# Optimization experiments

Measured on AMD Instinct MI355X. Metric: run time of the kernel, lower is better.

The kernel has to match this reference:

```python
import jax, jax.numpy as jnp
import numpy as np

N_NODES = 100000
N_EDGES = 1600000
D_INPUT = 128
D_HIDDEN = 16
N_HEADS = 8
NCLASSES = 40
N_GRAPHS = 64
ALPHA = 0.2  # LeakyReLU negative slope
INIT = 0.01  # GAT_param_init uniform range


def setup_inputs() -> dict:
    key = jax.random.key(0)
    ks = jax.random.split(key, 7)
    x = jax.random.normal(ks[0], (N_NODES, D_INPUT), dtype=jnp.float32)
    edge_idx = jax.random.randint(ks[1], (2, N_EDGES), 0, N_NODES, dtype=jnp.int64)
    batch = jnp.sort(jax.random.randint(ks[2], (N_NODES,), 0, N_GRAPHS, dtype=jnp.int64))
    # layer1: d_input -> n_heads * d_hidden, concat aggregate
    W1 = jax.random.uniform(ks[3], (D_INPUT, N_HEADS * D_HIDDEN), dtype=jnp.float32, minval=-INIT, maxval=INIT)
    a1 = jax.random.uniform(ks[4], (N_HEADS, 2 * D_HIDDEN), dtype=jnp.float32, minval=-INIT, maxval=INIT)
    # layer2: n_heads*d_hidden -> nclasses, 1 head, mean aggregate
    W2 = jax.random.uniform(ks[5], (N_HEADS * D_HIDDEN, NCLASSES), dtype=jnp.float32, minval=-INIT, maxval=INIT)
    a2 = jax.random.uniform(ks[6], (1, 2 * NCLASSES), dtype=jnp.float32, minval=-INIT, maxval=INIT)
    return {"x": x, "W1": W1, "a1": a1, "W2": W2, "a2": a2, "edge_idx": edge_idx, "batch": batch}


def _gat_layer(x, W, a, n_heads, d_out, src, dst, aggregate):
    # x: [N, d_in]; W: [d_in, H*D]; a: [H, 2*D]
    n = x.shape[0]
    Wh = (x @ W).reshape(n, n_heads, d_out)                  # [N, H, D]
    e_src = jnp.einsum('nhd,hd->nh', Wh, a[:, :d_out])       # [N, H]
    e_dst = jnp.einsum('nhd,hd->nh', Wh, a[:, d_out:])       # [N, H]
    e = jax.nn.leaky_relu(e_src[src] + e_dst[dst], ALPHA)    # [E, H]
    # segment softmax over edges sharing the same destination node
    m = jax.ops.segment_max(e, dst, num_segments=n)          # [N, H]
    m = jnp.where(jnp.isfinite(m), m, 0.0)                   # nodes w/o in-edges
    ex = jnp.exp(e - m[dst])
    s = jax.ops.segment_sum(ex, dst, num_segments=n)
    att = ex / (s[dst] + 1e-16)                              # [E, H]
    # weighted scatter-aggregate of neighbor features
    out = jax.ops.segment_sum(att[:, :, None] * Wh[src], dst, num_segments=n)  # [N, H, D]
    if aggregate == 'concat':
        return out.reshape(n, n_heads * d_out)
    return out.mean(axis=1)


def reference(x, W1, a1, W2, a2, edge_idx, batch):
    # eval mode: F.dropout(training=False) is identity
    src, dst = edge_idx[0], edge_idx[1]
    h1 = _gat_layer(x, W1, a1, N_HEADS, D_HIDDEN, src, dst, 'concat')
    h1 = jax.nn.elu(h1)
    h2 = _gat_layer(h1, W2, a2, 1, NCLASSES, src, dst, 'mean')   # [N, nclasses]
    # global_mean_pool over graph ids
    sums = jax.ops.segment_sum(h2, batch, num_segments=N_GRAPHS)
    cnt = jax.ops.segment_sum(jnp.ones((h2.shape[0],), h2.dtype), batch, num_segments=N_GRAPHS)
    return sums / jnp.maximum(cnt, 1.0)[:, None]
```

## Files before the change

### kernel.cpp

```cpp
#include <hip/hip_runtime.h>
#include <hip/hip_bf16.h>

typedef unsigned short u16;
typedef unsigned int   u32;
typedef float f32x2 __attribute__((ext_vector_type(2)));
typedef float f32x4 __attribute__((ext_vector_type(4)));
typedef short bf16x8 __attribute__((ext_vector_type(8)));

static constexpr int NN = 100000;
static constexpr int NE = 1600000;
static constexpr int NG = 64;

static constexpr int BSH   = 8;
static constexpr int NBUCK = 391;
static constexpr int BCAP  = 5120;
static constexpr int PB    = 8;

__device__ __forceinline__ u16 bf16rte(float a) {
  u32 u = __builtin_bit_cast(u32, a);
  u = (u + 0x7FFFu + ((u >> 16) & 1u)) >> 16;
  return (u16)u;
}
__device__ __forceinline__ u32 bf16pair(float a, float b) {
  return (u32)bf16rte(a) | ((u32)bf16rte(b) << 16);
}
__device__ __forceinline__ float bflo(u32 u) { return __builtin_bit_cast(float, u << 16); }
__device__ __forceinline__ float bfhi(u32 u) { return __builtin_bit_cast(float, u & 0xFFFF0000u); }

__device__ __forceinline__ void pkfma(f32x2& a, f32x2 w2, u32 u) {
  f32x2 v;
  v.x = bflo(u); v.y = bfhi(u);
  asm("v_pk_fma_f32 %0, %1, %2, %0" : "+v"(a) : "v"(w2), "v"(v));
}

__global__ void k_prep(const float* __restrict__ W1, u16* __restrict__ wsTg,
                       const int* __restrict__ batch, int* __restrict__ gstart,
                       int* __restrict__ cur) {
  const int bid = blockIdx.x;
  if (bid < 64) {
    int idx = bid * 256 + threadIdx.x;
    int k = idx >> 7, c = idx & 127;
    wsTg[c * 128 + (((k >> 3) ^ (c & 7)) << 3) + (k & 7)] = bf16rte(W1[idx]);
  } else {
    int t = threadIdx.x;
    for (int i = t; i < NBUCK; i += 256) cur[i] = 0;
    if (t <= NG) {
      int lo = 0, hi = NN;
      while (lo < hi) { int mid = (lo + hi) >> 1; if (batch[mid] < t) lo = mid + 1; else hi = mid; }
      gstart[t] = lo;
    }
  }
}

__global__ __launch_bounds__(256) void k_gemm1(
    const float* __restrict__ x, const u16* __restrict__ wsTg, const float* __restrict__ a1,
    u16* __restrict__ Wh1b, float* __restrict__ es1, float* __restrict__ ed1)
{
  __shared__ u16 wsT[128][128];
  __shared__ u16 xsb[64][32];
  const int t = threadIdx.x;
  const int w = t >> 6, l = t & 63;
  const int rowBase = blockIdx.x * 64;

  {
    const uint4* src = (const uint4*)wsTg;
    uint4* dst = (uint4*)&wsT[0][0];
#pragma unroll
    for (int i = 0; i < 8; ++i) dst[t * 8 + i] = src[t * 8 + i];
  }

  f32x4 acc[4][2];
#pragma unroll
  for (int r = 0; r < 4; ++r)
#pragma unroll
    for (int cf = 0; cf < 2; ++cf) acc[r][cf] = (f32x4){0.f, 0.f, 0.f, 0.f};

  const int rr = t >> 2, cg = t & 3;
  const int grow_s = rowBase + rr;

  for (int kk0 = 0; kk0 < 128; kk0 += 32) {
    float4 v0 = make_float4(0.f, 0.f, 0.f, 0.f), v1 = v0;
    if (grow_s < NN) {
      v0 = *(const float4*)(&x[(size_t)grow_s * 128 + kk0 + cg * 8]);
      v1 = *(const float4*)(&x[(size_t)grow_s * 128 + kk0 + cg * 8 + 4]);
    }
    if (kk0) __syncthreads();
    {
      u32 p0 = bf16pair(v0.x, v0.y);
      u32 p1 = bf16pair(v0.z, v0.w);
      u32 p2 = bf16pair(v1.x, v1.y);
      u32 p3 = bf16pair(v1.z, v1.w);
      int sg = cg ^ ((rr >> 1) & 3);
      *(uint4*)(&xsb[rr][sg * 8]) = make_uint4(p0, p1, p2, p3);
    }
    __syncthreads();

    bf16x8 bfr[2];
#pragma unroll
    for (int cf = 0; cf < 2; ++cf) {
      int col = w * 32 + cf * 16 + (l & 15);
      int kg = (kk0 >> 3) + (l >> 4);
      bfr[cf] = *(const bf16x8*)(&wsT[col][(kg ^ (col & 7)) * 8]);
    }
#pragma unroll
    for (int r = 0; r < 4; ++r) {
      int row = r * 16 + (l & 15);
      int kg = l >> 4;
      bf16x8 afr = *(const bf16x8*)(&xsb[row][(kg ^ ((row >> 1) & 3)) * 8]);
#pragma unroll
      for (int cf = 0; cf < 2; ++cf)
        acc[r][cf] = __builtin_amdgcn_mfma_f32_16x16x32_bf16(afr, bfr[cf], acc[r][cf], 0, 0, 0);
    }
  }

  const int cl = l & 15;
  const int rq = l >> 4;
#pragma unroll
  for (int cf = 0; cf < 2; ++cf) {
    const int h = w * 2 + cf;
    const int gcol = w * 32 + cf * 16 + cl;
    const float as = a1[h * 32 + cl];
    const float ad = a1[h * 32 + 16 + cl];
#pragma unroll
    for (int r = 0; r < 4; ++r) {
#pragma unroll
      for (int i = 0; i < 4; ++i) {
        int grow = rowBase + r * 16 + rq * 4 + i;
        float wh = acc[r][cf][i];
        float ps = wh * as, pd = wh * ad;
        ps += __shfl_xor(ps, 1); ps += __shfl_xor(ps, 2);
        ps += __shfl_xor(ps, 4); ps += __shfl_xor(ps, 8);
        pd += __shfl_xor(pd, 1); pd += __shfl_xor(pd, 2);
        pd += __shfl_xor(pd, 4); pd += __shfl_xor(pd, 8);
        if (grow < NN) {
          Wh1b[(size_t)grow * 128 + gcol] = bf16rte(wh);
          if (cl == 0) { es1[grow * 8 + h] = ps; ed1[grow * 8 + h] = pd; }
        }
      }
    }
  }
}

__global__ __launch_bounds__(256) void k_bin(
    const int* __restrict__ src, const int* __restrict__ dst,
    int* __restrict__ cur, u32* __restrict__ ebuf)
{
  __shared__ int lcnt2[2][512];
  __shared__ int scn[512];
  __shared__ int goff[NBUCK];
  const int t = threadIdx.x;
  const int wp = (t >> 7) & 1;
  const int e0 = blockIdx.x * 4096;

  lcnt2[0][t] = 0; lcnt2[0][t + 256] = 0;
  lcnt2[1][t] = 0; lcnt2[1][t + 256] = 0;
  __syncthreads();

  u32 ent[16]; short bb[16], lp[16];
#pragma unroll
  for (int i = 0; i < 16; ++i) {
    int e = e0 + i * 256 + t;
    if (e < NE) {
      int s = src[e], d = dst[e];
      int b = d >> BSH;
      ent[i] = (u32)s | ((u32)(d & 255) << 20);
      bb[i] = (short)b;
      lp[i] = (short)atomicAdd(&lcnt2[wp][b], 1);
    } else bb[i] = -1;
  }
  __syncthreads();
  scn[t] = lcnt2[0][t] + lcnt2[1][t];
  scn[t + 256] = lcnt2[0][t + 256] + lcnt2[1][t + 256];
  __syncthreads();
  for (int d = 1; d < 512; d <<= 1) {
    int v0 = (t >= d) ? scn[t - d] : 0;
    int v1 = (t + 256 >= d) ? scn[t + 256 - d] : 0;
    __syncthreads();
    scn[t] += v0; scn[t + 256] += v1;
    __syncthreads();
  }
  for (int b = t; b < NBUCK; b += 256) {
    int excl = b ? scn[b - 1] : 0;
    int cnt = scn[b] - excl;
    if (cnt) goff[b] = b * BCAP + atomicAdd(&cur[b], cnt);
  }
  __syncthreads();
#pragma unroll
  for (int i = 0; i < 16; ++i) {
    if (bb[i] >= 0) {
      int b = bb[i];
      int g = goff[b] + (wp ? lcnt2[0][b] : 0) + lp[i];
      if (g < (b + 1) * BCAP) ebuf[g] = ent[i];
    }
  }
}

__global__ __launch_bounds__(256) void k_sort(
    const int* __restrict__ cur, u32* __restrict__ ebuf,
    int* __restrict__ offs, int* __restrict__ deg)
{
  __shared__ u32 ein[BCAP];
  __shared__ u32 eout[BCAP];
  __shared__ int nd[256];
  __shared__ int ncur[256];
  const int t = threadIdx.x;
  const int b = blockIdx.x;
  const int base = b * BCAP;
  int cnt = cur[b];
  if (cnt > BCAP) cnt = BCAP;
  const int nloc = min(256, NN - (b << BSH));

  for (int i = t; i < cnt; i += 256) ein[i] = ebuf[base + i];
  nd[t] = 0;
  __syncthreads();
  for (int i = t; i < cnt; i += 256) atomicAdd(&nd[ein[i] >> 20], 1);
  __syncthreads();
  const int myCnt = nd[t];
  for (int d = 1; d < 256; d <<= 1) {
    int v = (t >= d) ? nd[t - d] : 0;
    __syncthreads();
    nd[t] += v;
    __syncthreads();
  }
  const int excl = t ? nd[t - 1] : 0;
  ncur[t] = excl;
  if (t < nloc) {
    int node = (b << BSH) + t;
    offs[node] = base + excl;
    deg[node]  = myCnt;
  }
  __syncthreads();
  for (int i = t; i < cnt; i += 256) {
    u32 v = ein[i];
    int pos = atomicAdd(&ncur[v >> 20], 1);
    eout[pos] = v & 0xFFFFFu;
  }
  __syncthreads();
  for (int i = t; i < cnt; i += 256) ebuf[base + i] = eout[i];
}

__global__ __launch_bounds__(256, 8) void k_agg1(
    const u16* __restrict__ Wh1b, const float* __restrict__ es1, const float* __restrict__ ed1,
    const int* __restrict__ offs, const int* __restrict__ deg, const int* __restrict__ csr,
    u16* __restrict__ h1b)
{
  const int wid = threadIdx.x >> 6;
  const int lane = threadIdx.x & 63;
  const int n = blockIdx.x * 4 + wid;
  if (n >= NN) return;
  const int s0 = offs[n];
  const int nE = deg[n];
  const int g = lane >> 4;
  const int db = lane & 15;
  const int h = db >> 1;
  const float edv = ed1[n * 8 + h];

  f32x2 acc[4];
#pragma unroll
  for (int i = 0; i < 4; ++i) { acc[i].x = 0.f; acc[i].y = 0.f; }
  float ssum = 0.f;

  int c0 = 0;
  for (; c0 + 16 <= nE; c0 += 16) {
    int ss[4];
#pragma unroll
    for (int q = 0; q < 4; ++q) ss[q] = csr[s0 + c0 + q * 4 + g];
    float zz[4];
#pragma unroll
    for (int q = 0; q < 4; ++q) {
      float z = es1[ss[q] * 8 + h] + edv;
      zz[q] = (z > 0.f) ? z : 0.2f * z;
    }
    uint4 raw[4];
#pragma unroll
    for (int q = 0; q < 4; ++q)
      raw[q] = *(const uint4*)(Wh1b + (size_t)ss[q] * 128 + db * 8);
#pragma unroll
    for (int q = 0; q < 4; ++q) {
      const float ww = __expf(zz[q]);
      ssum += ww;
      f32x2 w2; w2.x = ww; w2.y = ww;
      pkfma(acc[0], w2, raw[q].x);
      pkfma(acc[1], w2, raw[q].y);
      pkfma(acc[2], w2, raw[q].z);
      pkfma(acc[3], w2, raw[q].w);
    }
  }
  if (c0 < nE) {
    int jj[4], ss[4];
#pragma unroll
    for (int q = 0; q < 4; ++q) {
      jj[q] = c0 + q * 4 + g;
      ss[q] = csr[s0 + (jj[q] < nE ? jj[q] : 0)];
    }
    float zz[4];
#pragma unroll
    for (int q = 0; q < 4; ++q) {
      float z = es1[ss[q] * 8 + h] + edv;
      zz[q] = (z > 0.f) ? z : 0.2f * z;
    }
#pragma unroll
    for (int q = 0; q < 4; ++q) {
      if (jj[q] < nE) {
        const uint4 raw = *(const uint4*)(Wh1b + (size_t)ss[q] * 128 + db * 8);
        const float ww = __expf(zz[q]);
        ssum += ww;
        f32x2 w2; w2.x = ww; w2.y = ww;
        pkfma(acc[0], w2, raw.x);
        pkfma(acc[1], w2, raw.y);
        pkfma(acc[2], w2, raw.z);
        pkfma(acc[3], w2, raw.w);
      }
    }
  }
#pragma unroll
  for (int i = 0; i < 4; ++i) {
    acc[i].x += __shfl_xor(acc[i].x, 16);
    acc[i].y += __shfl_xor(acc[i].y, 16);
    acc[i].x += __shfl_xor(acc[i].x, 32);
    acc[i].y += __shfl_xor(acc[i].y, 32);
  }
  ssum += __shfl_xor(ssum, 16);
  ssum += __shfl_xor(ssum, 32);

  if (g == 0) {
    float inv = 1.f / (ssum + 1e-16f);
    float o[8];
#pragma unroll
    for (int i = 0; i < 4; ++i) {
      float v0 = acc[i].x * inv;
      float v1 = acc[i].y * inv;
      o[2 * i]     = (v0 > 0.f) ? v0 : expm1f(v0);
      o[2 * i + 1] = (v1 > 0.f) ? v1 : expm1f(v1);
    }
    u32 p0 = bf16pair(o[0], o[1]);
    u32 p1 = bf16pair(o[2], o[3]);
    u32 p2 = bf16pair(o[4], o[5]);
    u32 p3 = bf16pair(o[6], o[7]);
    *(uint4*)(h1b + (size_t)n * 128 + db * 8) = make_uint4(p0, p1, p2, p3);
  }
}

__global__ __launch_bounds__(256) void k_gemm2(
    const u16* __restrict__ h1b, const float* __restrict__ W2,
    const float* __restrict__ a2,
    u16* __restrict__ Wh2b, float* __restrict__ es2, float* __restrict__ ed2)
{
  __shared__ float hs[128][36];
  __shared__ float w2s[32][40];
  const int t = threadIdx.x;
  const int rowBase = blockIdx.x * 128;
  const int cg = t & 3;
  const int rs = t >> 2;
  float acc[2][10];
#pragma unroll
  for (int r = 0; r < 2; ++r)
#pragma unroll
    for (int j = 0; j < 10; ++j) acc[r][j] = 0.f;

  for (int k0 = 0; k0 < 128; k0 += 32) {
#pragma unroll
    for (int p = 0; p < 2; ++p) {
      int idx = (p * 256 + t) * 8;
      int rr = idx >> 5, cc = idx & 31;
      int grow = rowBase + rr;
      uint4 hv = make_uint4(0u, 0u, 0u, 0u);
      if (grow < NN) hv = *(const uint4*)(h1b + (size_t)grow * 128 + k0 + cc);
      float2* dst = (float2*)&hs[rr][cc];
      dst[0] = make_float2(bflo(hv.x), bfhi(hv.x));
      dst[1] = make_float2(bflo(hv.y), bfhi(hv.y));
      dst[2] = make_float2(bflo(hv.z), bfhi(hv.z));
      dst[3] = make_float2(bflo(hv.w), bfhi(hv.w));
    }
#pragma unroll
    for (int p = 0; p < 5; ++p) {
      int idx = p * 256 + t;
      int kk = idx / 40, cc = idx % 40;
      w2s[kk][cc] = W2[(size_t)(k0 + kk) * 40 + cc];
    }
    __syncthreads();
#pragma unroll
    for (int k = 0; k < 32; ++k) {
      float a0 = hs[rs][k], a1v = hs[rs + 64][k];
#pragma unroll
      for (int j = 0; j < 10; ++j) {
        float b = w2s[k][cg * 10 + j];
        acc[0][j] = fmaf(a0, b, acc[0][j]);
        acc[1][j] = fmaf(a1v, b, acc[1][j]);
      }
    }
    __syncthreads();
  }
  float a2s[10], a2d[10];
#pragma unroll
  for (int j = 0; j < 10; ++j) {
    a2s[j] = a2[cg * 10 + j];
    a2d[j] = a2[40 + cg * 10 + j];
  }
#pragma unroll
  for (int rr = 0; rr < 2; ++rr) {
    int grow = rowBase + rs + rr * 64;
    float pes = 0.f, ped = 0.f;
#pragma unroll
    for (int j = 0; j < 10; ++j) {
      float v = acc[rr][j];
      pes = fmaf(v, a2s[j], pes);
      ped = fmaf(v, a2d[j], ped);
    }
    if (grow < NN) {
      u32* dst = (u32*)(Wh2b + (size_t)grow * 48 + cg * 10);
      dst[0] = bf16pair(acc[rr][0], acc[rr][1]);
      dst[1] = bf16pair(acc[rr][2], acc[rr][3]);
      dst[2] = bf16pair(acc[rr][4], acc[rr][5]);
      dst[3] = bf16pair(acc[rr][6], acc[rr][7]);
      dst[4] = bf16pair(acc[rr][8], acc[rr][9]);
    }
    pes += __shfl_xor(pes, 1); pes += __shfl_xor(pes, 2);
    ped += __shfl_xor(ped, 1); ped += __shfl_xor(ped, 2);
    if (cg == 0 && grow < NN) { es2[grow] = pes; ed2[grow] = ped; }
  }
}

__global__ __launch_bounds__(256, 8) void k_agg2(
    const u16* __restrict__ Wh2b, const float* __restrict__ es2, const float* __restrict__ ed2,
    const int* __restrict__ offs, const int* __restrict__ deg, const int* __restrict__ csr,
    u32* __restrict__ h2b)
{
  __shared__ float red[4][64][5];
  const int wid = threadIdx.x >> 6;
  const int lane = threadIdx.x & 63;
  const int n = blockIdx.x * 4 + wid;
  if (n >= NN) return;
  const int s0 = offs[n];
  const int nE = deg[n];
  const float edv = ed2[n];
  int e6 = lane / 10;
  const int r10 = lane - e6 * 10;
  const bool act = lane < 60;
  if (e6 > 5) e6 = 5;

  f32x2 acc0, acc1;
  acc0.x = acc0.y = acc1.x = acc1.y = 0.f;
  float ssum = 0.f;

  for (int c0 = 0; c0 < nE; c0 += 24) {
    int jj[4], ss[4];
#pragma unroll
    for (int q = 0; q < 4; ++q) {
      jj[q] = c0 + q * 6 + e6;
      ss[q] = csr[s0 + (jj[q] < nE ? jj[q] : 0)];
    }
    float zz[4];
#pragma unroll
    for (int q = 0; q < 4; ++q) {
      float z = es2[ss[q]] + edv;
      zz[q] = (z > 0.f) ? z : 0.2f * z;
    }
#pragma unroll
    for (int q = 0; q < 4; ++q) {
      if (act && jj[q] < nE) {
        const uint2 raw = *(const uint2*)(Wh2b + (size_t)ss[q] * 48 + r10 * 4);
        const float ww = __expf(zz[q]);
        ssum += ww;
        f32x2 w2; w2.x = ww; w2.y = ww;
        pkfma(acc0, w2, raw.x);
        pkfma(acc1, w2, raw.y);
      }
    }
  }
  red[wid][lane][0] = acc0.x; red[wid][lane][1] = acc0.y;
  red[wid][lane][2] = acc1.x; red[wid][lane][3] = acc1.y;
  red[wid][lane][4] = ssum;
  __builtin_amdgcn_wave_barrier();
  if (lane < 20) {
    const int rb = lane >> 1;
    const int eA = (lane & 1) * 2;
    float aA = 0.f, aB = 0.f, sm = 0.f;
#pragma unroll
    for (int g = 0; g < 6; ++g) {
      aA += red[wid][g * 10 + rb][eA];
      aB += red[wid][g * 10 + rb][eA + 1];
      sm += red[wid][g * 10][4];
    }
    float inv = 1.f / (sm + 1e-16f);
    h2b[(size_t)n * 20 + lane] = bf16pair(aA * inv, aB * inv);
  }
}

__global__ __launch_bounds__(256) void k_pool1(
    const u32* __restrict__ h2b, const int* __restrict__ gstart,
    float* __restrict__ partial)
{
  __shared__ float lds[25][10][4];
  const int g = blockIdx.x >> 3;
  const int p = blockIdx.x & 7;
  const int t = threadIdx.x;
  const int s0 = gstart[g], s1 = gstart[g + 1];
  const int len = s1 - s0;
  const int chunk = (len + PB - 1) / PB;
  const int start = s0 + p * chunk;
  const int end = min(start + chunk, s1);
  const int slot = t / 10, q = t - slot * 10;
  float4 acc = make_float4(0.f, 0.f, 0.f, 0.f);
  if (slot < 25) {
    for (int n = start + slot; n < end; n += 25) {
      const uint2 v = *(const uint2*)(&h2b[(size_t)n * 20 + q * 2]);
      acc.x += bflo(v.x); acc.y += bfhi(v.x);
      acc.z += bflo(v.y); acc.w += bfhi(v.y);
    }
    lds[slot][q][0] = acc.x; lds[slot][q][1] = acc.y;
    lds[slot][q][2] = acc.z; lds[slot][q][3] = acc.w;
  }
  __syncthreads();
  if (t < 40) {
    const int qq = t >> 2, e = t & 3;
    float s = 0.f;
#pragma unroll
    for (int sl = 0; sl < 25; ++sl) s += lds[sl][qq][e];
    partial[(size_t)blockIdx.x * 40 + t] = s;
  }
}

__global__ void k_pool2(const float* __restrict__ partial, const int* __restrict__ gstart,
                        float* __restrict__ out)
{
  const int g = blockIdx.x;
  const int d = threadIdx.x;
  if (d >= 40) return;
  float s = 0.f;
#pragma unroll
  for (int p = 0; p < PB; ++p) s += partial[(size_t)(g * PB + p) * 40 + d];
  int cnt = gstart[g + 1] - gstart[g];
  if (cnt < 1) cnt = 1;
  out[g * 40 + d] = s / (float)cnt;
}

extern "C" void kernel_launch(void* const* d_in, const int* in_sizes, int n_in,
                              void* d_out, int out_size, void* d_ws, size_t ws_size,
                              hipStream_t stream)
{
  const float* x   = (const float*)d_in[0];
  const float* W1  = (const float*)d_in[1];
  const float* a1  = (const float*)d_in[2];
  const float* W2  = (const float*)d_in[3];
  const float* a2  = (const float*)d_in[4];
  const int* eidx  = (const int*)d_in[5];
  const int* batch = (const int*)d_in[6];
  float* out = (float*)d_out;

  char* ws = (char*)d_ws;
  u16*   Wh1b = (u16*)(ws + 0);
  u16*   Wh2b = (u16*)(ws + 0);
  u32*   h2b  = (u32*)(ws + 9600000);
  u16*   h1b  = (u16*)(ws + 25600000);
  float* es1  = (float*)(ws + 51200000);
  float* ed1  = (float*)(ws + 54400000);
  float* es2  = (float*)(ws + 57600000);
  float* ed2  = (float*)(ws + 58000000);
  u32*   ebuf = (u32*)(ws + 58400000);
  int*   offs = (int*)(ws + 66407680);
  int*   deg  = (int*)(ws + 66807680);
  int*   cur  = (int*)(ws + 67207680);
  int*   gstart = (int*)(ws + 67209728);
  float* partial = (float*)(ws + 67210240);
  u16*   wsTg = (u16*)(ws + 67292160);

  const int* esrc = eidx;
  const int* edst = eidx + NE;

  k_prep<<<65, 256, 0, stream>>>(W1, wsTg, batch, gstart, cur);
  k_gemm1<<<(NN + 63) / 64, 256, 0, stream>>>(x, wsTg, a1, Wh1b, es1, ed1);
  k_bin<<<(NE + 4095) / 4096, 256, 0, stream>>>(esrc, edst, cur, ebuf);
  k_sort<<<NBUCK, 256, 0, stream>>>(cur, ebuf, offs, deg);
  k_agg1<<<(NN + 3) / 4, 256, 0, stream>>>(Wh1b, es1, ed1, offs, deg, (const int*)ebuf, h1b);
  k_gemm2<<<(NN + 127) / 128, 256, 0, stream>>>(h1b, W2, a2, Wh2b, es2, ed2);
  k_agg2<<<(NN + 3) / 4, 256, 0, stream>>>(Wh2b, es2, ed2, offs, deg, (const int*)ebuf, h2b);
  k_pool1<<<NG * PB, 256, 0, stream>>>(h2b, gstart, partial);
  k_pool2<<<NG, 64, 0, stream>>>(partial, gstart, out);
}
```

Before: 245.1 us.

## Fuse layer-2 projection into layer-1 aggregation kernel via LDS-resident W2

Merges the layer-1 aggregation with the layer-2 GEMM. Each wave now applies ELU to its node's aggregated features in registers and immediately multiplies them by a bf16-packed W2 staged in shared memory. It then reduces across lanes to produce Wh2, es2 and ed2 directly. This removes the bf16 h1 intermediate's global write and re-read, plus one kernel launch. In exchange, every block reloads 10 KB of packed W2 into LDS, and the occupancy hint on the fused kernel is relaxed.

Result: faster. 238.4 us (median of 2 runs) (-2.7%).

```diff
diff --git a/kernel.cpp b/kernel.cpp
--- a/kernel.cpp
+++ b/kernel.cpp
@@ -35,19 +35,28 @@
 
 __global__ void k_prep(const float* __restrict__ W1, u16* __restrict__ wsTg,
                        const int* __restrict__ batch, int* __restrict__ gstart,
-                       int* __restrict__ cur) {
+                       int* __restrict__ cur,
+                       const float* __restrict__ W2, u32* __restrict__ wsW2) {
   const int bid = blockIdx.x;
   if (bid < 64) {
     int idx = bid * 256 + threadIdx.x;
     int k = idx >> 7, c = idx & 127;
     wsTg[c * 128 + (((k >> 3) ^ (c & 7)) << 3) + (k & 7)] = bf16rte(W1[idx]);
-  } else {
+  } else if (bid == 64) {
     int t = threadIdx.x;
     for (int i = t; i < NBUCK; i += 256) cur[i] = 0;
     if (t <= NG) {
       int lo = 0, hi = NN;
       while (lo < hi) { int mid = (lo + hi) >> 1; if (batch[mid] < t) lo = mid + 1; else hi = mid; }
       gstart[t] = lo;
+    }
+  } else {
+    const int t = threadIdx.x;
+#pragma unroll
+    for (int i = 0; i < 10; ++i) {
+      int idx = t * 10 + i;
+      int pc = idx >> 7, d = idx & 127;
+      wsW2[idx] = bf16pair(W2[d * 40 + pc * 2], W2[d * 40 + pc * 2 + 1]);
     }
   }
 }
@@ -239,13 +248,20 @@
   for (int i = t; i < cnt; i += 256) ebuf[base + i] = eout[i];
 }
 
-__global__ __launch_bounds__(256, 8) void k_agg1(
+__global__ __launch_bounds__(256) void k_agg1g2(
     const u16* __restrict__ Wh1b, const float* __restrict__ es1, const float* __restrict__ ed1,
     const int* __restrict__ offs, const int* __restrict__ deg, const int* __restrict__ csr,
-    u16* __restrict__ h1b)
-{
-  const int wid = threadIdx.x >> 6;
-  const int lane = threadIdx.x & 63;
+    const u32* __restrict__ wsW2, const float* __restrict__ a2,
+    u16* __restrict__ Wh2b, float* __restrict__ es2, float* __restrict__ ed2)
+{
+  __shared__ u32 W2s[2560];
+  const int t = threadIdx.x;
+#pragma unroll
+  for (int i = 0; i < 10; ++i) W2s[t * 10 + i] = wsW2[t * 10 + i];
+  __syncthreads();
+
+  const int wid = t >> 6;
+  const int lane = t & 63;
   const int n = blockIdx.x * 4 + wid;
   if (n >= NN) return;
   const int s0 = offs[n];
@@ -323,101 +339,53 @@
   ssum += __shfl_xor(ssum, 16);
   ssum += __shfl_xor(ssum, 32);
 
-  if (g == 0) {
-    float inv = 1.f / (ssum + 1e-16f);
-    float o[8];
-#pragma unroll
-    for (int i = 0; i < 4; ++i) {
-      float v0 = acc[i].x * inv;
-      float v1 = acc[i].y * inv;
-      o[2 * i]     = (v0 > 0.f) ? v0 : expm1f(v0);
-      o[2 * i + 1] = (v1 > 0.f) ? v1 : expm1f(v1);
-    }
-    u32 p0 = bf16pair(o[0], o[1]);
-    u32 p1 = bf16pair(o[2], o[3]);
-    u32 p2 = bf16pair(o[4], o[5]);
-    u32 p3 = bf16pair(o[6], o[7]);
-    *(uint4*)(h1b + (size_t)n * 128 + db * 8) = make_uint4(p0, p1, p2, p3);
-  }
-}
-
-__global__ __launch_bounds__(256) void k_gemm2(
-    const u16* __restrict__ h1b, const float* __restrict__ W2,
-    const float* __restrict__ a2,
-    u16* __restrict__ Wh2b, float* __restrict__ es2, float* __restrict__ ed2)
-{
-  __shared__ float hs[128][36];
-  __shared__ float w2s[32][40];
-  const int t = threadIdx.x;
-  const int rowBase = blockIdx.x * 128;
-  const int cg = t & 3;
-  const int rs = t >> 2;
-  float acc[2][10];
-#pragma unroll
-  for (int r = 0; r < 2; ++r)
-#pragma unroll
-    for (int j = 0; j < 10; ++j) acc[r][j] = 0.f;
-
-  for (int k0 = 0; k0 < 128; k0 += 32) {
-#pragma unroll
-    for (int p = 0; p < 2; ++p) {
-      int idx = (p * 256 + t) * 8;
-      int rr = idx >> 5, cc = idx & 31;
-      int grow = rowBase + rr;
-      uint4 hv = make_uint4(0u, 0u, 0u, 0u);
-      if (grow < NN) hv = *(const uint4*)(h1b + (size_t)grow * 128 + k0 + cc);
-      float2* dst = (float2*)&hs[rr][cc];
-      dst[0] = make_float2(bflo(hv.x), bfhi(hv.x));
-      dst[1] = make_float2(bflo(hv.y), bfhi(hv.y));
-      dst[2] = make_float2(bflo(hv.z), bfhi(hv.z));
-      dst[3] = make_float2(bflo(hv.w), bfhi(hv.w));
-    }
+  const float inv = 1.f / (ssum + 1e-16f);
+  float hv[8];
+#pragma unroll
+  for (int i = 0; i < 4; ++i) {
+    float v0 = acc[i].x * inv;
+    float v1 = acc[i].y * inv;
+    hv[2 * i]     = (v0 > 0.f) ? v0 : expm1f(v0);
+    hv[2 * i + 1] = (v1 > 0.f) ? v1 : expm1f(v1);
+  }
+
+  float o[10];
+#pragma unroll
+  for (int j = 0; j < 10; ++j) o[j] = 0.f;
+#pragma unroll
+  for (int d = 0; d < 8; ++d) {
+    const float hvd = hv[d];
+    const int row = db * 8 + d;
 #pragma unroll
     for (int p = 0; p < 5; ++p) {
-      int idx = p * 256 + t;
-      int kk = idx / 40, cc = idx % 40;
-      w2s[kk][cc] = W2[(size_t)(k0 + kk) * 40 + cc];
-    }
-    __syncthreads();
-#pragma unroll
-    for (int k = 0; k < 32; ++k) {
-      float a0 = hs[rs][k], a1v = hs[rs + 64][k];
-#pragma unroll
-      for (int j = 0; j < 10; ++j) {
-        float b = w2s[k][cg * 10 + j];
-        acc[0][j] = fmaf(a0, b, acc[0][j]);
-        acc[1][j] = fmaf(a1v, b, acc[1][j]);
-      }
-    }
-    __syncthreads();
-  }
-  float a2s[10], a2d[10];
+      u32 pr = W2s[(g * 5 + p) * 128 + row];
+      o[2 * p]     = fmaf(hvd, bflo(pr), o[2 * p]);
+      o[2 * p + 1] = fmaf(hvd, bfhi(pr), o[2 * p + 1]);
+    }
+  }
 #pragma unroll
   for (int j = 0; j < 10; ++j) {
-    a2s[j] = a2[cg * 10 + j];
-    a2d[j] = a2[40 + cg * 10 + j];
-  }
-#pragma unroll
-  for (int rr = 0; rr < 2; ++rr) {
-    int grow = rowBase + rs + rr * 64;
+    o[j] += __shfl_xor(o[j], 1);
+    o[j] += __shfl_xor(o[j], 2);
+    o[j] += __shfl_xor(o[j], 4);
+    o[j] += __shfl_xor(o[j], 8);
+  }
+  if (db == 0) {
+    u32* dst = (u32*)(Wh2b + (size_t)n * 48 + g * 10);
+    dst[0] = bf16pair(o[0], o[1]);
+    dst[1] = bf16pair(o[2], o[3]);
+    dst[2] = bf16pair(o[4], o[5]);
+    dst[3] = bf16pair(o[6], o[7]);
+    dst[4] = bf16pair(o[8], o[9]);
     float pes = 0.f, ped = 0.f;
 #pragma unroll
     for (int j = 0; j < 10; ++j) {
-      float v = acc[rr][j];
-      pes = fmaf(v, a2s[j], pes);
-      ped = fmaf(v, a2d[j], ped);
-    }
-    if (grow < NN) {
-      u32* dst = (u32*)(Wh2b + (size_t)grow * 48 + cg * 10);
-      dst[0] = bf16pair(acc[rr][0], acc[rr][1]);
-      dst[1] = bf16pair(acc[rr][2], acc[rr][3]);
-      dst[2] = bf16pair(acc[rr][4], acc[rr][5]);
-      dst[3] = bf16pair(acc[rr][6], acc[rr][7]);
-      dst[4] = bf16pair(acc[rr][8], acc[rr][9]);
-    }
-    pes += __shfl_xor(pes, 1); pes += __shfl_xor(pes, 2);
-    ped += __shfl_xor(ped, 1); ped += __shfl_xor(ped, 2);
-    if (cg == 0 && grow < NN) { es2[grow] = pes; ed2[grow] = ped; }
+      pes = fmaf(o[j], a2[g * 10 + j], pes);
+      ped = fmaf(o[j], a2[40 + g * 10 + j], ped);
+    }
+    pes += __shfl_xor(pes, 16); pes += __shfl_xor(pes, 32);
+    ped += __shfl_xor(ped, 16); ped += __shfl_xor(ped, 32);
+    if (lane == 0) { es2[n] = pes; ed2[n] = ped; }
   }
 }
 
@@ -550,9 +518,8 @@
 
   char* ws = (char*)d_ws;
   u16*   Wh1b = (u16*)(ws + 0);
-  u16*   Wh2b = (u16*)(ws + 0);
   u32*   h2b  = (u32*)(ws + 9600000);
-  u16*   h1b  = (u16*)(ws + 25600000);
+  u16*   Wh2b = (u16*)(ws + 25600000);
   float* es1  = (float*)(ws + 51200000);
   float* ed1  = (float*)(ws + 54400000);
   float* es2  = (float*)(ws + 57600000);
@@ -564,16 +531,17 @@
   int*   gstart = (int*)(ws + 67209728);
   float* partial = (float*)(ws + 67210240);
   u16*   wsTg = (u16*)(ws + 67292160);
+  u32*   wsW2 = (u32*)(ws + 67324928);
 
   const int* esrc = eidx;
   const int* edst = eidx + NE;
 
-  k_prep<<<65, 256, 0, stream>>>(W1, wsTg, batch, gstart, cur);
+  k_prep<<<66, 256, 0, stream>>>(W1, wsTg, batch, gstart, cur, W2, wsW2);
   k_gemm1<<<(NN + 63) / 64, 256, 0, stream>>>(x, wsTg, a1, Wh1b, es1, ed1);
   k_bin<<<(NE + 4095) / 4096, 256, 0, stream>>>(esrc, edst, cur, ebuf);
   k_sort<<<NBUCK, 256, 0, stream>>>(cur, ebuf, offs, deg);
-  k_agg1<<<(NN + 3) / 4, 256, 0, stream>>>(Wh1b, es1, ed1, offs, deg, (const int*)ebuf, h1b);
-  k_gemm2<<<(NN + 127) / 128, 256, 0, stream>>>(h1b, W2, a2, Wh2b, es2, ed2);
+  k_agg1g2<<<(NN + 3) / 4, 256, 0, stream>>>(Wh1b, es1, ed1, offs, deg, (const int*)ebuf,
+                                             wsW2, a2, Wh2b, es2, ed2);
   k_agg2<<<(NN + 3) / 4, 256, 0, stream>>>(Wh2b, es2, ed2, offs, deg, (const int*)ebuf, h2b);
   k_pool1<<<NG * PB, 256, 0, stream>>>(h2b, gstart, partial);
   k_pool2<<<NG, 64, 0, stream>>>(partial, gstart, out);
```
